# Kernel optimization log

Measured on AMD Instinct MI355X. Metric: run time of the kernel, lower is better.

Reference implementation:

```python
import jax, jax.numpy as jnp
import numpy as np

N = 2048
D_T = 256; D_F = 256
E_T = 32; E_F = 32; E_C = 128
C = 5; Q = 512


def setup_inputs() -> dict:
    key = jax.random.key(0)
    ks = jax.random.split(key, 12)
    # full graph minus self-loops, row-major (matches dense_to_sparse ordering)
    r, c = np.meshgrid(np.arange(N), np.arange(N), indexing='ij')
    m = r != c
    edge_index = jnp.asarray(np.stack([r[m], c[m]]), dtype=jnp.int32)  # [2, N*(N-1)]
    E = edge_index.shape[1]
    s = 0.02
    return {
        'time_features': jax.random.normal(ks[0], (N, D_T), jnp.float32),
        'edge_index': edge_index,
        'time_edge_weight': jax.random.uniform(ks[1], (E,), jnp.float32),
        'freq_features': jax.random.normal(ks[2], (N, D_F), jnp.float32),
        'freq_edge_weight': jax.random.uniform(ks[3], (E,), jnp.float32),
        'labels': jax.random.randint(ks[4], (N,), 0, C, jnp.int32),
        'num_classes': C,
        'query_size': Q,
        'Wt': jax.random.normal(ks[5], (D_T, E_T), jnp.float32) * s,
        'bt': jnp.zeros((E_T,), jnp.float32),
        'Wf': jax.random.normal(ks[6], (D_F, E_F), jnp.float32) * s,
        'bf': jnp.zeros((E_F,), jnp.float32),
        'Wc': jax.random.normal(ks[7], (E_T + E_F + C, E_C), jnp.float32) * s,
        'bc': jnp.zeros((E_C,), jnp.float32),
        'Wo': jax.random.normal(ks[8], (E_C, C), jnp.float32) * s,
        'bo': jnp.zeros((C,), jnp.float32),
    }


def _gcn(x, A, W, b):
    # torch_geometric GCNConv: D^{-1/2}(A + I)D^{-1/2} (X W) + b
    n = A.shape[0]
    Ah = A + jnp.eye(n, dtype=A.dtype)
    deg = Ah.sum(axis=1)
    dis = jnp.where(deg > 0, jax.lax.rsqrt(deg), 0.0)
    return (dis[:, None] * Ah * dis[None, :]) @ (x @ W) + b


def reference(time_features, edge_index, time_edge_weight, freq_features,
              freq_edge_weight, labels, num_classes, query_size,
              Wt, bt, Wf, bf, Wc, bc, Wo, bo):
    n = time_features.shape[0]
    lrelu = lambda z: jax.nn.leaky_relu(z, 0.01)

    def dense_adj(w):  # A[dst, src] = w
        return jnp.zeros((n, n), w.dtype).at[edge_index[1], edge_index[0]].add(w)

    te = lrelu(_gcn(time_features, dense_adj(time_edge_weight), Wt, bt))
    fe = lrelu(_gcn(freq_features, dense_adj(freq_edge_weight), Wf, bf))

    # to_one_hot: one_hot[:n - query_size, labels] = 1 -> support rows get 1 in
    # every column that appears anywhere in `labels`
    cols = jnp.zeros((num_classes,), te.dtype).at[labels].set(1.0)
    rowmask = (jnp.arange(n) < (n - query_size)).astype(te.dtype)
    one_hot = rowmask[:, None] * cols[None, :]

    feats = jnp.concatenate([te, fe, one_hot], axis=-1)  # [n, E_T+E_F+C]

    # graph_construction (no_grad in original): 1 / (L1 distance over the
    # non-one-hot dims + 1e-5), zero diagonal
    fd = jax.lax.stop_gradient(feats[:, : feats.shape[1] - num_classes])
    dist = jnp.sum(jnp.abs(fd[:, None, :] - fd[None, :, :]), axis=-1)  # [n, n]
    Aw = (1.0 / (dist + 1e-5)) * (1.0 - jnp.eye(n, dtype=feats.dtype))

    emb = lrelu(_gcn(feats, Aw, Wc, bc))
    return emb @ Wo + bo
```

## Files before the change

### kernel.cpp

```cpp
#include <hip/hip_runtime.h>
#include <hip/hip_bf16.h>

#define N 2048
#define NM1 2047
#define DT 256
#define ET 32
#define EC 128
#define NC 5
#define FS 80
#define FD 69
#define KC_ET 16
#define KC_EC 16

typedef __hip_bfloat16 bf16;

__global__ __launch_bounds__(256) void k_deg_label(const float* __restrict__ tw,
                                                   const float* __restrict__ fw,
                                                   const int* __restrict__ labels,
                                                   float* __restrict__ degT,
                                                   float* __restrict__ degF,
                                                   float* __restrict__ cols){
    int b = blockIdx.x;
    int t = threadIdx.x;
    if (b == 512){
        __shared__ float lc[NC];
        if (t < NC) lc[t] = 0.f;
        __syncthreads();
        for (int i = t; i < N; i += 256){
            int l = labels[i];
            if (l >= 0 && l < NC) lc[l] = 1.f;
        }
        __syncthreads();
        if (t < NC) cols[t] = lc[t];
        return;
    }
    int p = (b & 7)*256 + t;
    if (p >= NM1) return;
    int s0 = (b >> 3)*32;
    float lowT=0.f, highT=0.f, lowF=0.f, highF=0.f;
    #pragma unroll 8
    for (int r = 0; r < 32; ++r){
        int s = s0 + r;
        float vt = tw[(size_t)s*NM1 + p];
        float vf = fw[(size_t)s*NM1 + p];
        if (s <= p){ highT += vt; highF += vf; }
        else       { lowT  += vt; lowF  += vf; }
    }
    atomicAdd(&degT[p],   lowT);
    atomicAdd(&degF[p],   lowF);
    atomicAdd(&degT[p+1], highT);
    atomicAdd(&degF[p+1], highF);
}

__global__ __launch_bounds__(256) void k_xw(const float* __restrict__ Xt,
                                            const float* __restrict__ Wt,
                                            float* __restrict__ Yt,
                                            const float* __restrict__ Xf,
                                            const float* __restrict__ Wf,
                                            float* __restrict__ Yf){
    const float* X = blockIdx.y ? Xf : Xt;
    const float* W = blockIdx.y ? Wf : Wt;
    float*       Y = blockIdx.y ? Yf : Yt;
    __shared__ float Ws[DT*ET];
    __shared__ float Xs[8*DT];
    int t = threadIdx.x;
    for (int idx = t; idx < DT*ET; idx += 256) Ws[idx] = W[idx];
    int i0 = blockIdx.x*8;
    for (int idx = t; idx < 8*DT; idx += 256) Xs[idx] = X[(size_t)i0*DT + idx];
    __syncthreads();
    int r = t >> 5, f = t & 31;
    const float* xr = Xs + r*DT;
    float acc = 0.f;
    #pragma unroll 8
    for (int d = 0; d < DT; ++d) acc += xr[d]*Ws[d*ET+f];
    Y[(size_t)(i0+r)*ET+f] = acc;
}

__global__ __launch_bounds__(256) void k_agg_et(const float* __restrict__ tw,
                                                const float* __restrict__ fw,
                                                const float* __restrict__ Yt,
                                                const float* __restrict__ Yf,
                                                const float* __restrict__ degT,
                                                const float* __restrict__ degF,
                                                float* __restrict__ Pt,
                                                float* __restrict__ Pf){
    __shared__ float Ast[64*68];
    __shared__ float Asf[64*68];
    __shared__ float Zst[64*ET];
    __shared__ float Zsf[64*ET];
    int t = threadIdx.x;
    int i0 = blockIdx.x*64;
    int kc = blockIdx.y;
    int k0 = kc*128;
    int g  = t >> 7;
    int tt = t & 127;
    int ig = tt >> 3, fg = tt & 7;
    int r0 = ig*4, c0 = fg*4;
    const float* As = g ? Asf : Ast;
    const float* Zs = g ? Zsf : Zst;
    float acc[4][4];
    #pragma unroll
    for (int u=0;u<4;++u)
        #pragma unroll
        for (int v=0;v<4;++v) acc[u][v]=0.f;

    for (int kt = 0; kt < 2; ++kt){
        int kb = k0 + kt*64;
        #pragma unroll
        for (int e = 0; e < 16; ++e){
            int id = t + e*256;
            int k_l = id >> 6, i_l = id & 63;
            int k = kb + k_l;
            int gi = i0 + i_l;
            float vt, vf;
            if (gi == k){ vt = 0.f; vf = 0.f; }
            else {
                size_t base = (size_t)k*NM1 + gi - (gi > k ? 1 : 0);
                vt = tw[base]; vf = fw[base];
            }
            Ast[k_l*68 + i_l] = vt;
            Asf[k_l*68 + i_l] = vf;
        }
        #pragma unroll
        for (int e = 0; e < 2; ++e){
            int id = t + e*256;
            int row = id >> 3;
            int c4  = (id & 7)*4;
            float rdT = rsqrtf(1.f + degT[kb+row]);
            float rdF = rsqrtf(1.f + degF[kb+row]);
            float4 yt = *(const float4*)&Yt[(size_t)(kb+row)*ET + c4];
            float4 yf = *(const float4*)&Yf[(size_t)(kb+row)*ET + c4];
            yt.x*=rdT; yt.y*=rdT; yt.z*=rdT; yt.w*=rdT;
            yf.x*=rdF; yf.y*=rdF; yf.z*=rdF; yf.w*=rdF;
            *(float4*)&Zst[row*ET + c4] = yt;
            *(float4*)&Zsf[row*ET + c4] = yf;
        }
        __syncthreads();
        for (int k = 0; k < 64; ++k){
            float4 a = *(const float4*)&As[k*68 + r0];
            float4 z = *(const float4*)&Zs[k*ET + c0];
            const float* ap = (const float*)&a;
            const float* zp = (const float*)&z;
            #pragma unroll
            for (int u = 0; u < 4; ++u)
                #pragma unroll
                for (int v = 0; v < 4; ++v)
                    acc[u][v] += ap[u]*zp[v];
        }
        __syncthreads();
    }
    float* P = g ? Pf : Pt;
    #pragma unroll
    for (int u = 0; u < 4; ++u){
        size_t ii = (size_t)(i0 + r0 + u);
        float4 o;
        float* po = (float*)&o;
        #pragma unroll
        for (int v = 0; v < 4; ++v) po[v]=acc[u][v];
        *(float4*)&P[(size_t)kc*(N*ET) + ii*ET + c0] = o;
    }
}

__global__ __launch_bounds__(256) void k_feats_epi(const float* __restrict__ Pt,
                                                   const float* __restrict__ Pf,
                                                   const float* __restrict__ Yt,
                                                   const float* __restrict__ Yf,
                                                   const float* __restrict__ degT,
                                                   const float* __restrict__ degF,
                                                   const float* __restrict__ bt,
                                                   const float* __restrict__ bfv,
                                                   const float* __restrict__ cols,
                                                   const int* __restrict__ qsize,
                                                   float* __restrict__ feats){
    int idx = blockIdx.x*256 + threadIdx.x;
    int i = idx >> 6;
    int f = idx & 63;
    float s, rd, b;
    if (f < ET){
        rd = rsqrtf(1.f + degT[i]);
        s = rd*Yt[(size_t)i*ET + f];
        #pragma unroll
        for (int kc = 0; kc < KC_ET; ++kc) s += Pt[(size_t)kc*(N*ET) + (size_t)i*ET + f];
        b = bt[f];
    } else {
        int g = f - ET;
        rd = rsqrtf(1.f + degF[i]);
        s = rd*Yf[(size_t)i*ET + g];
        #pragma unroll
        for (int kc = 0; kc < KC_ET; ++kc) s += Pf[(size_t)kc*(N*ET) + (size_t)i*ET + g];
        b = bfv[g];
    }
    float v = rd*s + b;
    feats[(size_t)i*FS + f] = v > 0.f ? v : 0.01f*v;
    if (f < NC){
        int nsup = N - qsize[0];
        feats[(size_t)i*FS + 2*ET + f] = (i < nsup) ? cols[f] : 0.f;
    }
}

__global__ __launch_bounds__(256) void k_build_aw(const float* __restrict__ feats,
                                                  float* __restrict__ Aw,
                                                  float* __restrict__ dsum){
    int bi = blockIdx.x, bj = blockIdx.y;
    if (bi > bj) return;
    __shared__ float fiT[64*68];
    __shared__ float fjT[64*68];
    int t = threadIdx.x;
    int i0 = bi*64, j0 = bj*64;
    {
        int row = t >> 2;
        int cb  = (t & 3)*16;
        const float4* si = (const float4*)(feats + (size_t)(i0+row)*FS + cb);
        const float4* sj = (const float4*)(feats + (size_t)(j0+row)*FS + cb);
        #pragma unroll
        for (int s = 0; s < 4; ++s){
            float4 v = si[s];
            float4 w = sj[s];
            int c = cb + s*4;
            fiT[(c+0)*68+row]=v.x; fiT[(c+1)*68+row]=v.y; fiT[(c+2)*68+row]=v.z; fiT[(c+3)*68+row]=v.w;
            fjT[(c+0)*68+row]=w.x; fjT[(c+1)*68+row]=w.y; fjT[(c+2)*68+row]=w.z; fjT[(c+3)*68+row]=w.w;
        }
    }
    __syncthreads();
    int tx = t & 15, ty = t >> 4;
    float acc[4][4];
    #pragma unroll
    for (int u=0;u<4;++u)
        #pragma unroll
        for (int v=0;v<4;++v) acc[u][v]=0.f;
    for (int d = 0; d < 64; ++d){
        float4 a4 = *(const float4*)&fiT[d*68 + ty*4];
        float4 b4 = *(const float4*)&fjT[d*68 + tx*4];
        const float* ap = (const float*)&a4;
        const float* bp = (const float*)&b4;
        #pragma unroll
        for (int u = 0; u < 4; ++u)
            #pragma unroll
            for (int v = 0; v < 4; ++v)
                acc[u][v] += fabsf(ap[u]-bp[v]);
    }
    bool offdiag = (bi != bj);
    float cs[4] = {0.f,0.f,0.f,0.f};
    #pragma unroll
    for (int u = 0; u < 4; ++u){
        int gi = i0 + ty*4 + u;
        float4 o;
        float* po = (float*)&o;
        #pragma unroll
        for (int v = 0; v < 4; ++v){
            int gj = j0 + tx*4 + v;
            po[v] = (gi==gj) ? 1.0f : 1.0f/(acc[u][v] + 1e-5f);
        }
        *(float4*)&Aw[(size_t)gi*N + j0 + tx*4] = o;
        if (offdiag){
            #pragma unroll
            for (int v = 0; v < 4; ++v){
                int gj = j0 + tx*4 + v;
                Aw[(size_t)gj*N + gi] = po[v];
                cs[v] += po[v];
            }
        }
        float rs = (po[0]+po[1]) + (po[2]+po[3]);
        rs += __shfl_xor(rs, 1);
        rs += __shfl_xor(rs, 2);
        rs += __shfl_xor(rs, 4);
        rs += __shfl_xor(rs, 8);
        if (tx == 0) atomicAdd(&dsum[gi], rs);
    }
    if (offdiag){
        #pragma unroll
        for (int v = 0; v < 4; ++v){
            cs[v] += __shfl_xor(cs[v], 16);
            cs[v] += __shfl_xor(cs[v], 32);
        }
        if ((t & 48) == 0){
            #pragma unroll
            for (int v = 0; v < 4; ++v)
                atomicAdd(&dsum[j0 + tx*4 + v], cs[v]);
        }
    }
}

__global__ __launch_bounds__(256) void k_featswc(const float* __restrict__ feats,
                                                 const float* __restrict__ Wc,
                                                 const float* __restrict__ dsum,
                                                 float* __restrict__ Zc){
    __shared__ float Wcs[FD*EC];
    __shared__ float fr[8][FD+3];
    int t = threadIdx.x;
    for (int idx = t; idx < FD*EC; idx += 256) Wcs[idx] = Wc[idx];
    int i0 = blockIdx.x*8;
    for (int idx = t; idx < 8*FD; idx += 256){
        int r = idx / FD;
        int c = idx - r*FD;
        fr[r][c] = feats[(size_t)(i0+r)*FS + c];
    }
    __syncthreads();
    int f  = t & 127;
    int rh = t >> 7;
    for (int rr = 0; rr < 4; ++rr){
        int r = rh*4 + rr;
        float acc = 0.f;
        #pragma unroll
        for (int d = 0; d < FD; ++d) acc += fr[r][d]*Wcs[d*EC+f];
        int i = i0 + r;
        Zc[(size_t)i*EC + f] = rsqrtf(dsum[i])*acc;
    }
}

__global__ __launch_bounds__(256) void k_agg_ec(const float* __restrict__ Aw,
                                                const float* __restrict__ Zc,
                                                float* __restrict__ Pe){
    __shared__ float As[64*128];
    __shared__ float Zs[64*128];
    int t = threadIdx.x;
    int i0 = blockIdx.x*128;
    int kc = blockIdx.y;
    int k0 = kc*128;
    int rg = t >> 4;
    int cg = t & 15;
    int r0 = rg*8;
    int ca = cg*4, cb = 64 + cg*4;
    float acc[8][8];
    #pragma unroll
    for (int u=0;u<8;++u)
        #pragma unroll
        for (int v=0;v<8;++v) acc[u][v]=0.f;

    for (int kt = 0; kt < 2; ++kt){
        int kb = k0 + kt*64;
        #pragma unroll
        for (int e = 0; e < 8; ++e){
            int id = t + e*256;
            int k_l = id >> 5;
            int i4  = (id & 31)*4;
            *(float4*)&As[k_l*128 + i4] = *(const float4*)&Aw[(size_t)(kb+k_l)*N + i0 + i4];
        }
        #pragma unroll
        for (int e = 0; e < 8; ++e){
            int id = t + e*256;
            int row = id >> 5;
            int c4  = (id & 31)*4;
            *(float4*)&Zs[row*128 + c4] = *(const float4*)&Zc[(size_t)(kb+row)*EC + c4];
        }
        __syncthreads();
        for (int k = 0; k < 64; ++k){
            float4 a0 = *(const float4*)&As[k*128 + r0];
            float4 a1 = *(const float4*)&As[k*128 + r0 + 4];
            float4 z0 = *(const float4*)&Zs[k*128 + ca];
            float4 z1 = *(const float4*)&Zs[k*128 + cb];
            float a8[8] = {a0.x,a0.y,a0.z,a0.w,a1.x,a1.y,a1.z,a1.w};
            float zl[4] = {z0.x,z0.y,z0.z,z0.w};
            float zh[4] = {z1.x,z1.y,z1.z,z1.w};
            #pragma unroll
            for (int u = 0; u < 8; ++u){
                #pragma unroll
                for (int v = 0; v < 4; ++v){
                    acc[u][v]   += a8[u]*zl[v];
                    acc[u][v+4] += a8[u]*zh[v];
                }
            }
        }
        __syncthreads();
    }
    #pragma unroll
    for (int u = 0; u < 8; ++u){
        size_t ii = (size_t)(i0 + r0 + u);
        float4 o0, o1;
        float* p0 = (float*)&o0; float* p1 = (float*)&o1;
        #pragma unroll
        for (int v = 0; v < 4; ++v){ p0[v]=acc[u][v]; p1[v]=acc[u][v+4]; }
        *(float4*)&Pe[(size_t)kc*(N*EC) + ii*EC + ca] = o0;
        *(float4*)&Pe[(size_t)kc*(N*EC) + ii*EC + cb] = o1;
    }
}

__global__ __launch_bounds__(256) void k_embfinal(const float* __restrict__ Pe,
                                                  const float* __restrict__ dsum,
                                                  const float* __restrict__ bc,
                                                  const float* __restrict__ Wo,
                                                  const float* __restrict__ bo,
                                                  float* __restrict__ out){
    __shared__ float vs[2][EC];
    __shared__ float Wos[EC*NC];
    __shared__ float bos[NC];
    int t = threadIdx.x;
    for (int idx = t; idx < EC*NC; idx += 256) Wos[idx] = Wo[idx];
    if (t < NC) bos[t] = bo[t];
    int rr = t >> 7, f = t & 127;
    int i = blockIdx.x*2 + rr;
    size_t idx = (size_t)i*EC + f;
    float s = 0.f;
    #pragma unroll
    for (int kc = 0; kc < KC_EC; ++kc) s += Pe[(size_t)kc*(N*EC) + idx];
    float v = rsqrtf(dsum[i])*s + bc[f];
    vs[rr][f] = v > 0.f ? v : 0.01f*v;
    __syncthreads();
    if (t < 2*NC){
        int r = t / NC;
        int c = t - r*NC;
        float a = bos[c];
        #pragma unroll 8
        for (int f2 = 0; f2 < EC; ++f2) a += vs[r][f2]*Wos[f2*NC+c];
        out[(size_t)(blockIdx.x*2 + r)*NC + c] = a;
    }
}

extern "C" void kernel_launch(void* const* d_in, const int* in_sizes, int n_in,
                              void* d_out, int out_size, void* d_ws, size_t ws_size,
                              hipStream_t stream) {
    const float* time_features = (const float*)d_in[0];
    const float* tw            = (const float*)d_in[2];
    const float* freq_features = (const float*)d_in[3];
    const float* fw            = (const float*)d_in[4];
    const int*   labels        = (const int*)d_in[5];
    const int*   qsize         = (const int*)d_in[7];
    const float* Wt  = (const float*)d_in[8];
    const float* bt  = (const float*)d_in[9];
    const float* Wf  = (const float*)d_in[10];
    const float* bfv = (const float*)d_in[11];
    const float* Wc  = (const float*)d_in[12];
    const float* bc  = (const float*)d_in[13];
    const float* Wo  = (const float*)d_in[14];
    const float* bo  = (const float*)d_in[15];
    float* out = (float*)d_out;

    float* ws    = (float*)d_ws;
    float* Yt    = ws;
    float* Yf    = Yt + (size_t)N*ET;
    float* Zc    = Yf + (size_t)N*ET;
    float* degT  = Zc + (size_t)N*EC;
    float* degF  = degT + N;
    float* dsum  = degF + N;
    float* colsb = dsum + N;
    float* feats = colsb + 8;
    float* Aw    = feats + (size_t)N*FS;
    float* Pt    = Aw + (size_t)N*N;
    float* Pf    = Pt + (size_t)KC_ET*N*ET;
    float* Pe    = Pf + (size_t)KC_ET*N*ET;

    hipMemsetAsync(degT, 0, 3*N*sizeof(float), stream);
    k_xw<<<dim3(N/8, 2), 256, 0, stream>>>(time_features, Wt, Yt,
                                           freq_features, Wf, Yf);
    k_deg_label<<<513, 256, 0, stream>>>(tw, fw, labels, degT, degF, colsb);
    k_agg_et<<<dim3(N/64, KC_ET), 256, 0, stream>>>(tw, fw, Yt, Yf, degT, degF, Pt, Pf);
    k_feats_epi<<<(N*64)/256, 256, 0, stream>>>(Pt, Pf, Yt, Yf, degT, degF,
                                                bt, bfv, colsb, qsize, feats);
    k_build_aw<<<dim3(N/64, N/64), 256, 0, stream>>>(feats, Aw, dsum);
    k_featswc<<<N/8, 256, 0, stream>>>(feats, Wc, dsum, Zc);
    k_agg_ec<<<dim3(N/128, KC_EC), 256, 0, stream>>>(Aw, Zc, Pe);
    k_embfinal<<<N/2, 256, 0, stream>>>(Pe, dsum, bc, Wo, bo, out);
}
```

Before: 216.5 us.

## Fuse degree and XW kernels, drop Aw symmetry, load full K tile in agg_ec

Merges the degree/label kernel and the X@W projection into one launch so that one kernel launch disappears and the two independent workloads can overlap. The distance-matrix builder now computes every 64x64 tile directly instead of only the upper triangle with a mirrored transpose write, which removes the strided transposed stores and column atomics at the cost of twice the distance arithmetic. The edge-aggregation GEMM now loads a 128-deep K slab into 128 KB of shared memory in one pass rather than two 64-deep passes, removing one barrier pair but greatly raising LDS use and reducing occupancy.

```diff
diff --git a/kernel.cpp b/kernel.cpp
--- a/kernel.cpp
+++ b/kernel.cpp
@@ -14,14 +14,39 @@
 
 typedef __hip_bfloat16 bf16;
 
-__global__ __launch_bounds__(256) void k_deg_label(const float* __restrict__ tw,
-                                                   const float* __restrict__ fw,
-                                                   const int* __restrict__ labels,
-                                                   float* __restrict__ degT,
-                                                   float* __restrict__ degF,
-                                                   float* __restrict__ cols){
+__global__ __launch_bounds__(256) void k_deg_label_xw(const float* __restrict__ tw,
+                                                      const float* __restrict__ fw,
+                                                      const int* __restrict__ labels,
+                                                      const float* __restrict__ Xt,
+                                                      const float* __restrict__ Wt,
+                                                      const float* __restrict__ Xf,
+                                                      const float* __restrict__ Wf,
+                                                      float* __restrict__ degT,
+                                                      float* __restrict__ degF,
+                                                      float* __restrict__ cols,
+                                                      float* __restrict__ Yt,
+                                                      float* __restrict__ Yf){
     int b = blockIdx.x;
     int t = threadIdx.x;
+    if (b < 512){
+        int p = (b & 7)*256 + t;
+        if (p >= NM1) return;
+        int s0 = (b >> 3)*32;
+        float lowT=0.f, highT=0.f, lowF=0.f, highF=0.f;
+        #pragma unroll 8
+        for (int r = 0; r < 32; ++r){
+            int s = s0 + r;
+            float vt = tw[(size_t)s*NM1 + p];
+            float vf = fw[(size_t)s*NM1 + p];
+            if (s <= p){ highT += vt; highF += vf; }
+            else       { lowT  += vt; lowF  += vf; }
+        }
+        atomicAdd(&degT[p],   lowT);
+        atomicAdd(&degF[p],   lowF);
+        atomicAdd(&degT[p+1], highT);
+        atomicAdd(&degF[p+1], highF);
+        return;
+    }
     if (b == 512){
         __shared__ float lc[NC];
         if (t < NC) lc[t] = 0.f;
@@ -34,39 +59,15 @@
         if (t < NC) cols[t] = lc[t];
         return;
     }
-    int p = (b & 7)*256 + t;
-    if (p >= NM1) return;
-    int s0 = (b >> 3)*32;
-    float lowT=0.f, highT=0.f, lowF=0.f, highF=0.f;
-    #pragma unroll 8
-    for (int r = 0; r < 32; ++r){
-        int s = s0 + r;
-        float vt = tw[(size_t)s*NM1 + p];
-        float vf = fw[(size_t)s*NM1 + p];
-        if (s <= p){ highT += vt; highF += vf; }
-        else       { lowT  += vt; lowF  += vf; }
-    }
-    atomicAdd(&degT[p],   lowT);
-    atomicAdd(&degF[p],   lowF);
-    atomicAdd(&degT[p+1], highT);
-    atomicAdd(&degF[p+1], highF);
-}
-
-__global__ __launch_bounds__(256) void k_xw(const float* __restrict__ Xt,
-                                            const float* __restrict__ Wt,
-                                            float* __restrict__ Yt,
-                                            const float* __restrict__ Xf,
-                                            const float* __restrict__ Wf,
-                                            float* __restrict__ Yf){
-    const float* X = blockIdx.y ? Xf : Xt;
-    const float* W = blockIdx.y ? Wf : Wt;
-    float*       Y = blockIdx.y ? Yf : Yt;
+    int idx = b - 513;
+    const float* X = (idx & 256) ? Xf : Xt;
+    const float* W = (idx & 256) ? Wf : Wt;
+    float*       Y = (idx & 256) ? Yf : Yt;
     __shared__ float Ws[DT*ET];
     __shared__ float Xs[8*DT];
-    int t = threadIdx.x;
-    for (int idx = t; idx < DT*ET; idx += 256) Ws[idx] = W[idx];
-    int i0 = blockIdx.x*8;
-    for (int idx = t; idx < 8*DT; idx += 256) Xs[idx] = X[(size_t)i0*DT + idx];
+    for (int j = t; j < DT*ET; j += 256) Ws[j] = W[j];
+    int i0 = (idx & 255)*8;
+    for (int j = t; j < 8*DT; j += 256) Xs[j] = X[(size_t)i0*DT + j];
     __syncthreads();
     int r = t >> 5, f = t & 31;
     const float* xr = Xs + r*DT;
@@ -201,12 +202,10 @@
 __global__ __launch_bounds__(256) void k_build_aw(const float* __restrict__ feats,
                                                   float* __restrict__ Aw,
                                                   float* __restrict__ dsum){
-    int bi = blockIdx.x, bj = blockIdx.y;
-    if (bi > bj) return;
     __shared__ float fiT[64*68];
     __shared__ float fjT[64*68];
     int t = threadIdx.x;
-    int i0 = bi*64, j0 = bj*64;
+    int i0 = blockIdx.x*64, j0 = blockIdx.y*64;
     {
         int row = t >> 2;
         int cb  = (t & 3)*16;
@@ -239,8 +238,6 @@
             for (int v = 0; v < 4; ++v)
                 acc[u][v] += fabsf(ap[u]-bp[v]);
     }
-    bool offdiag = (bi != bj);
-    float cs[4] = {0.f,0.f,0.f,0.f};
     #pragma unroll
     for (int u = 0; u < 4; ++u){
         int gi = i0 + ty*4 + u;
@@ -252,14 +249,6 @@
             po[v] = (gi==gj) ? 1.0f : 1.0f/(acc[u][v] + 1e-5f);
         }
         *(float4*)&Aw[(size_t)gi*N + j0 + tx*4] = o;
-        if (offdiag){
-            #pragma unroll
-            for (int v = 0; v < 4; ++v){
-                int gj = j0 + tx*4 + v;
-                Aw[(size_t)gj*N + gi] = po[v];
-                cs[v] += po[v];
-            }
-        }
         float rs = (po[0]+po[1]) + (po[2]+po[3]);
         rs += __shfl_xor(rs, 1);
         rs += __shfl_xor(rs, 2);
@@ -267,18 +256,6 @@
         rs += __shfl_xor(rs, 8);
         if (tx == 0) atomicAdd(&dsum[gi], rs);
     }
-    if (offdiag){
-        #pragma unroll
-        for (int v = 0; v < 4; ++v){
-            cs[v] += __shfl_xor(cs[v], 16);
-            cs[v] += __shfl_xor(cs[v], 32);
-        }
-        if ((t & 48) == 0){
-            #pragma unroll
-            for (int v = 0; v < 4; ++v)
-                atomicAdd(&dsum[j0 + tx*4 + v], cs[v]);
-        }
-    }
 }
 
 __global__ __launch_bounds__(256) void k_featswc(const float* __restrict__ feats,
@@ -311,8 +288,8 @@
 __global__ __launch_bounds__(256) void k_agg_ec(const float* __restrict__ Aw,
                                                 const float* __restrict__ Zc,
                                                 float* __restrict__ Pe){
-    __shared__ float As[64*128];
-    __shared__ float Zs[64*128];
+    __shared__ float As[128*128];
+    __shared__ float Zs[128*128];
     int t = threadIdx.x;
     int i0 = blockIdx.x*128;
     int kc = blockIdx.y;
@@ -321,47 +298,45 @@
     int cg = t & 15;
     int r0 = rg*8;
     int ca = cg*4, cb = 64 + cg*4;
+
+    #pragma unroll
+    for (int e = 0; e < 16; ++e){
+        int id = t + e*256;
+        int k_l = id >> 5;
+        int i4  = (id & 31)*4;
+        *(float4*)&As[k_l*128 + i4] = *(const float4*)&Aw[(size_t)(k0+k_l)*N + i0 + i4];
+    }
+    #pragma unroll
+    for (int e = 0; e < 16; ++e){
+        int id = t + e*256;
+        int k_l = id >> 5;
+        int c4  = (id & 31)*4;
+        *(float4*)&Zs[k_l*128 + c4] = *(const float4*)&Zc[(size_t)(k0+k_l)*EC + c4];
+    }
+    __syncthreads();
+
     float acc[8][8];
     #pragma unroll
     for (int u=0;u<8;++u)
         #pragma unroll
         for (int v=0;v<8;++v) acc[u][v]=0.f;
 
-    for (int kt = 0; kt < 2; ++kt){
-        int kb = k0 + kt*64;
-        #pragma unroll
-        for (int e = 0; e < 8; ++e){
-            int id = t + e*256;
-            int k_l = id >> 5;
-            int i4  = (id & 31)*4;
-            *(float4*)&As[k_l*128 + i4] = *(const float4*)&Aw[(size_t)(kb+k_l)*N + i0 + i4];
-        }
-        #pragma unroll
-        for (int e = 0; e < 8; ++e){
-            int id = t + e*256;
-            int row = id >> 5;
-            int c4  = (id & 31)*4;
-            *(float4*)&Zs[row*128 + c4] = *(const float4*)&Zc[(size_t)(kb+row)*EC + c4];
-        }
-        __syncthreads();
-        for (int k = 0; k < 64; ++k){
-            float4 a0 = *(const float4*)&As[k*128 + r0];
-            float4 a1 = *(const float4*)&As[k*128 + r0 + 4];
-            float4 z0 = *(const float4*)&Zs[k*128 + ca];
-            float4 z1 = *(const float4*)&Zs[k*128 + cb];
-            float a8[8] = {a0.x,a0.y,a0.z,a0.w,a1.x,a1.y,a1.z,a1.w};
-            float zl[4] = {z0.x,z0.y,z0.z,z0.w};
-            float zh[4] = {z1.x,z1.y,z1.z,z1.w};
+    for (int k = 0; k < 128; ++k){
+        float4 a0 = *(const float4*)&As[k*128 + r0];
+        float4 a1 = *(const float4*)&As[k*128 + r0 + 4];
+        float4 z0 = *(const float4*)&Zs[k*128 + ca];
+        float4 z1 = *(const float4*)&Zs[k*128 + cb];
+        float a8[8] = {a0.x,a0.y,a0.z,a0.w,a1.x,a1.y,a1.z,a1.w};
+        float zl[4] = {z0.x,z0.y,z0.z,z0.w};
+        float zh[4] = {z1.x,z1.y,z1.z,z1.w};
+        #pragma unroll
+        for (int u = 0; u < 8; ++u){
             #pragma unroll
-            for (int u = 0; u < 8; ++u){
-                #pragma unroll
-                for (int v = 0; v < 4; ++v){
-                    acc[u][v]   += a8[u]*zl[v];
-                    acc[u][v+4] += a8[u]*zh[v];
-                }
+            for (int v = 0; v < 4; ++v){
+                acc[u][v]   += a8[u]*zl[v];
+                acc[u][v+4] += a8[u]*zh[v];
             }
         }
-        __syncthreads();
     }
     #pragma unroll
     for (int u = 0; u < 8; ++u){
@@ -440,9 +415,9 @@
     float* Pe    = Pf + (size_t)KC_ET*N*ET;
 
     hipMemsetAsync(degT, 0, 3*N*sizeof(float), stream);
-    k_xw<<<dim3(N/8, 2), 256, 0, stream>>>(time_features, Wt, Yt,
-                                           freq_features, Wf, Yf);
-    k_deg_label<<<513, 256, 0, stream>>>(tw, fw, labels, degT, degF, colsb);
+    k_deg_label_xw<<<1025, 256, 0, stream>>>(tw, fw, labels,
+                                             time_features, Wt, freq_features, Wf,
+                                             degT, degF, colsb, Yt, Yf);
     k_agg_et<<<dim3(N/64, KC_ET), 256, 0, stream>>>(tw, fw, Yt, Yf, degT, degF, Pt, Pf);
     k_feats_epi<<<(N*64)/256, 256, 0, stream>>>(Pt, Pf, Yt, Yf, degT, degF,
                                                 bt, bfv, colsb, qsize, feats);
```

Result: faster. 209.1 us (-3.4%).
